# Performance work log

Hardware: AMD Instinct MI355X
Metric: run time of the kernel (lower is better)

Reference implementation:

```python
import jax, jax.numpy as jnp
import numpy as np

NUM_Q = 500000
NUM_E = 250000
DIM = 256
HEADS = 4
NEG_SLOPE = 0.01
EPS = 1e-16


def setup_inputs() -> dict:
    key = jax.random.key(0)
    k1, k2, k3, k4, k5 = jax.random.split(key, 5)
    x_q = jax.random.normal(k1, (NUM_Q, DIM), dtype=jnp.float32)
    x_edge = jax.random.normal(k2, (NUM_E, DIM), dtype=jnp.float32)
    edge_ids = jax.random.randint(k3, (NUM_Q,), 0, NUM_E, dtype=jnp.int64)
    # learned params: w_q (input_dim, output_dim), attention weight (H, 2*dim/H)
    w_q = jax.random.normal(k4, (DIM, DIM), dtype=jnp.float32) / np.sqrt(DIM)
    weight = jax.random.normal(k5, (HEADS, 2 * DIM // HEADS), dtype=jnp.float32) / np.sqrt(2 * DIM // HEADS)
    return {"x_q": x_q, "x_edge": x_edge, "w_q": w_q, "weight": weight, "edge_ids": edge_ids}


def reference(x_q, x_edge, w_q, weight, edge_ids):
    nq = x_q.shape[0]
    ne = x_edge.shape[0]
    h = weight.shape[0]
    # project qualifier pairs: (nq, dim) -> (nq, H, d_head)
    xq = (x_q @ w_q).reshape(nq, h, -1)
    # gather edge reps per qualifier pair: (nq, H, d_head)
    xe = x_edge[edge_ids].reshape(nq, h, -1)
    # per-head attention logits: eh
    alpha = jnp.einsum('ehd,hd->eh', jnp.concatenate([xe, xq], axis=-1), weight)
    alpha = jax.nn.leaky_relu(alpha, NEG_SLOPE)
    # segment softmax grouped by edge_ids (numerically stable)
    seg_max = jax.ops.segment_max(alpha, edge_ids, num_segments=ne)
    seg_max = jnp.where(jnp.isfinite(seg_max), seg_max, 0.0)  # empty segments
    ex = jnp.exp(alpha - seg_max[edge_ids])
    seg_sum = jax.ops.segment_sum(ex, edge_ids, num_segments=ne)
    alpha = ex / (seg_sum[edge_ids] + EPS)
    # weight qualifier reps and scatter-add to edges
    xq = (alpha[..., None] * xq).reshape(nq, -1)
    return jax.ops.segment_sum(xq, edge_ids, num_segments=ne)
```

## Files before the change

kernel.cpp:

```cpp
#include <hip/hip_runtime.h>
#include <hip/hip_bf16.h>

#define DIM 256
#define HEADS 4
#define NEG_SLOPE 0.01f

typedef unsigned short u16;
typedef __attribute__((ext_vector_type(8))) short short8;
typedef __attribute__((ext_vector_type(4))) float f32x4;
typedef __attribute__((ext_vector_type(4))) unsigned short u16x4;

__device__ __forceinline__ u16 f2bf(float f) {
    unsigned u = __float_as_uint(f);
    unsigned r = (u + 0x7fffu + ((u >> 16) & 1u)) >> 16;
    return (u16)r;
}
__device__ __forceinline__ float bf2f(u16 h) {
    return __uint_as_float(((unsigned)h) << 16);
}

__global__ __launch_bounds__(256) void prepb_kernel(const float* __restrict__ B,
                                                    u16* __restrict__ BThi) {
    int k = blockIdx.x;
    int n = threadIdx.x;
    BThi[n * 256 + k] = f2bf(B[k * 256 + n]);
}

__global__ __launch_bounds__(256) void beta_kernel(const float* __restrict__ xe,
                                                   const float* __restrict__ weight,
                                                   float* __restrict__ beta, int NE) {
    int wid = blockIdx.x * 4 + (threadIdx.x >> 6);
    if (wid >= NE) return;
    int lane = threadIdx.x & 63;
    int h = lane >> 4;
    float4 v = *reinterpret_cast<const float4*>(xe + (size_t)wid * DIM + lane * 4);
    float4 w = *reinterpret_cast<const float4*>(weight + h * 128 + (lane & 15) * 4);
    float p = v.x * w.x + v.y * w.y + v.z * w.z + v.w * w.w;
    p += __shfl_xor(p, 1);
    p += __shfl_xor(p, 2);
    p += __shfl_xor(p, 4);
    p += __shfl_xor(p, 8);
    if ((lane & 15) == 0) beta[(size_t)wid * 4 + h] = p;
}

__global__ __launch_bounds__(256, 3) void gemm_fused_kernel(const float* __restrict__ A,
                                                            const u16* __restrict__ BThi,
                                                            const float* __restrict__ weight,
                                                            const float* __restrict__ beta,
                                                            const int* __restrict__ eids,
                                                            u16* __restrict__ xq_out,
                                                            float* __restrict__ exv,
                                                            float* __restrict__ segsum,
                                                            unsigned* __restrict__ counts,
                                                            int NQ) {
    __shared__ u16 Ahi_s[64 * 32];
    __shared__ u16 Bhi_s[256 * 32];

    const int t = threadIdx.x;
    const int lane = t & 63;
    const int wc = t >> 6;
    const int lr = lane & 15;
    const int kg = lane >> 4;
    const long brow = (long)blockIdx.x * 64;

    f32x4 acc[4][4];
#pragma unroll
    for (int m = 0; m < 4; ++m)
#pragma unroll
        for (int n = 0; n < 4; ++n) acc[m][n] = (f32x4){0.f, 0.f, 0.f, 0.f};

    for (int k0 = 0; k0 < DIM; k0 += 32) {
#pragma unroll
        for (int i = 0; i < 2; ++i) {
            int slot = t + i * 256;
            int row = slot >> 3, c4 = slot & 7;
            long grow = brow + row;
            if (grow >= NQ) grow = NQ - 1;
            float4 v = *reinterpret_cast<const float4*>(A + grow * DIM + k0 + c4 * 4);
            u16x4 hv;
            hv.x = f2bf(v.x); hv.y = f2bf(v.y); hv.z = f2bf(v.z); hv.w = f2bf(v.w);
            int swz = (c4 >> 1) ^ (row & 3) ^ ((row >> 2) & 3);
            int off = row * 32 + (swz << 3) + ((c4 & 1) << 2);
            *reinterpret_cast<u16x4*>(&Ahi_s[off]) = hv;
        }
#pragma unroll
        for (int i = 0; i < 4; ++i) {
            int slot = t + i * 256;
            int n = slot >> 2, c = slot & 3;
            uint4 vh = *reinterpret_cast<const uint4*>(BThi + n * 256 + k0 + c * 8);
            int swz = c ^ (n & 3) ^ ((n >> 2) & 3);
            *reinterpret_cast<uint4*>(&Bhi_s[n * 32 + (swz << 3)]) = vh;
        }
        __syncthreads();

        short8 bh[4];
#pragma unroll
        for (int n = 0; n < 4; ++n) {
            int nn = wc * 64 + n * 16 + lr;
            int off = nn * 32 + ((kg ^ (nn & 3) ^ ((nn >> 2) & 3)) << 3);
            bh[n] = *reinterpret_cast<const short8*>(&Bhi_s[off]);
        }
#pragma unroll
        for (int m = 0; m < 4; ++m) {
            int rr = m * 16 + lr;
            int off = rr * 32 + ((kg ^ (rr & 3) ^ ((rr >> 2) & 3)) << 3);
            short8 ah = *reinterpret_cast<const short8*>(&Ahi_s[off]);
#pragma unroll
            for (int n = 0; n < 4; ++n)
                acc[m][n] = __builtin_amdgcn_mfma_f32_16x16x32_bf16(ah, bh[n], acc[m][n], 0, 0, 0);
        }
        __syncthreads();
    }

    float wv[4];
#pragma unroll
    for (int n = 0; n < 4; ++n) wv[n] = weight[wc * 128 + 64 + n * 16 + lr];

#pragma unroll
    for (int m = 0; m < 4; ++m) {
#pragma unroll
        for (int r = 0; r < 4; ++r) {
            long row = brow + m * 16 + kg * 4 + r;
            bool ok = row < NQ;
            float p = 0.f;
#pragma unroll
            for (int n = 0; n < 4; ++n) {
                float v = acc[m][n][r];
                if (ok) xq_out[row * DIM + wc * 64 + n * 16 + lr] = f2bf(v);
                p = fmaf(v, wv[n], p);
            }
            p += __shfl_xor(p, 1);
            p += __shfl_xor(p, 2);
            p += __shfl_xor(p, 4);
            p += __shfl_xor(p, 8);
            if (ok && lr == 0) {
                int j = eids[row];
                float l = beta[(size_t)j * 4 + wc] + p;
                l = l > 0.f ? l : NEG_SLOPE * l;
                float e = __expf(l);
                exv[row * 4 + wc] = e;
                atomicAdd(&segsum[(size_t)j * 4 + wc], e);
                if (wc == 0) atomicAdd(&counts[j], 1u);
            }
        }
    }
}

__global__ __launch_bounds__(256) void scan1_kernel(const unsigned* __restrict__ counts,
                                                    unsigned* __restrict__ offs,
                                                    unsigned* __restrict__ blocksums, int NE) {
    __shared__ unsigned s[256];
    int t = threadIdx.x;
    int base = blockIdx.x * 1024 + t * 4;
    unsigned v[4], sum = 0;
#pragma unroll
    for (int i = 0; i < 4; ++i) {
        v[i] = (base + i < NE) ? counts[base + i] : 0u;
        sum += v[i];
    }
    s[t] = sum;
    __syncthreads();
    for (int off = 1; off < 256; off <<= 1) {
        unsigned y = (t >= off) ? s[t - off] : 0u;
        __syncthreads();
        s[t] += y;
        __syncthreads();
    }
    unsigned excl = s[t] - sum;
#pragma unroll
    for (int i = 0; i < 4; ++i) {
        if (base + i < NE) offs[base + i] = excl;
        excl += v[i];
    }
    if (t == 255) blocksums[blockIdx.x] = s[255];
}

__global__ __launch_bounds__(256) void scan2_kernel(unsigned* __restrict__ blocksums, int NB) {
    __shared__ unsigned s[256];
    int t = threadIdx.x;
    unsigned v = (t < NB) ? blocksums[t] : 0u;
    s[t] = v;
    __syncthreads();
    for (int off = 1; off < 256; off <<= 1) {
        unsigned y = (t >= off) ? s[t - off] : 0u;
        __syncthreads();
        s[t] += y;
        __syncthreads();
    }
    if (t < NB) blocksums[t] = s[t] - v;
}

__global__ __launch_bounds__(256) void scan3_kernel(unsigned* __restrict__ offs,
                                                    const unsigned* __restrict__ blocksums,
                                                    unsigned* __restrict__ cursor, int NE) {
    int t = threadIdx.x;
    int base = blockIdx.x * 1024 + t * 4;
    unsigned add = blocksums[blockIdx.x];
#pragma unroll
    for (int i = 0; i < 4; ++i) {
        if (base + i < NE) {
            unsigned o = offs[base + i] + add;
            offs[base + i] = o;
            cursor[base + i] = o;
        }
    }
}

__global__ __launch_bounds__(256) void fill_kernel(const int* __restrict__ eids,
                                                   unsigned* __restrict__ cursor,
                                                   int* __restrict__ qlist, int NQ) {
    int e = blockIdx.x * blockDim.x + threadIdx.x;
    if (e >= NQ) return;
    int j = eids[e];
    unsigned pos = atomicAdd(&cursor[j], 1u);
    qlist[pos] = e;
}

__global__ __launch_bounds__(256) void gather_kernel(const float* __restrict__ exv,
                                                     const float* __restrict__ segsum,
                                                     const unsigned* __restrict__ offs,
                                                     const unsigned* __restrict__ counts,
                                                     const int* __restrict__ qlist,
                                                     const u16* __restrict__ xq,
                                                     float* __restrict__ out, int NE) {
    int j = blockIdx.x * 4 + (threadIdx.x >> 6);
    if (j >= NE) return;
    int lane = threadIdx.x & 63;
    int h = lane >> 4;
    unsigned beg = offs[j];
    unsigned n = counts[j];
    float inv = 1.0f / (segsum[(size_t)j * 4 + h] + 1e-16f);
    float4 a0 = make_float4(0.f, 0.f, 0.f, 0.f);
    float4 a1 = make_float4(0.f, 0.f, 0.f, 0.f);
    unsigned i = 0;
    for (; i + 2 <= n; i += 2) {
        int q0 = qlist[beg + i];
        int q1 = qlist[beg + i + 1];
        float w0 = exv[(size_t)q0 * 4 + h] * inv;
        float w1 = exv[(size_t)q1 * 4 + h] * inv;
        u16x4 v0 = *reinterpret_cast<const u16x4*>(xq + (size_t)q0 * DIM + lane * 4);
        u16x4 v1 = *reinterpret_cast<const u16x4*>(xq + (size_t)q1 * DIM + lane * 4);
        a0.x = fmaf(w0, bf2f(v0.x), a0.x); a1.x = fmaf(w1, bf2f(v1.x), a1.x);
        a0.y = fmaf(w0, bf2f(v0.y), a0.y); a1.y = fmaf(w1, bf2f(v1.y), a1.y);
        a0.z = fmaf(w0, bf2f(v0.z), a0.z); a1.z = fmaf(w1, bf2f(v1.z), a1.z);
        a0.w = fmaf(w0, bf2f(v0.w), a0.w); a1.w = fmaf(w1, bf2f(v1.w), a1.w);
    }
    if (i < n) {
        int q0 = qlist[beg + i];
        float w0 = exv[(size_t)q0 * 4 + h] * inv;
        u16x4 v0 = *reinterpret_cast<const u16x4*>(xq + (size_t)q0 * DIM + lane * 4);
        a0.x = fmaf(w0, bf2f(v0.x), a0.x);
        a0.y = fmaf(w0, bf2f(v0.y), a0.y);
        a0.z = fmaf(w0, bf2f(v0.z), a0.z);
        a0.w = fmaf(w0, bf2f(v0.w), a0.w);
    }
    float4 acc = make_float4(a0.x + a1.x, a0.y + a1.y, a0.z + a1.z, a0.w + a1.w);
    *reinterpret_cast<float4*>(out + (size_t)j * DIM + lane * 4) = acc;
}

extern "C" void kernel_launch(void* const* d_in, const int* in_sizes, int n_in,
                              void* d_out, int out_size, void* d_ws, size_t ws_size,
                              hipStream_t stream) {
    (void)n_in; (void)out_size; (void)ws_size;
    const float* x_q    = (const float*)d_in[0];
    const float* x_edge = (const float*)d_in[1];
    const float* w_q    = (const float*)d_in[2];
    const float* weight = (const float*)d_in[3];
    const int*   eids   = (const int*)d_in[4];
    const int NQ = in_sizes[0] / DIM;
    const int NE = in_sizes[1] / DIM;
    float* out = (float*)d_out;

    u16*      xq        = (u16*)d_ws;
    float*    exv       = (float*)(xq + (size_t)NQ * DIM);
    float*    beta      = exv + (size_t)NQ * 4;
    float*    segsum    = beta + (size_t)NE * 4;
    unsigned* counts    = (unsigned*)(segsum + (size_t)NE * 4);
    unsigned* offs      = counts + NE;
    unsigned* cursor    = offs + NE;
    int*      qlist     = (int*)(cursor + NE);
    unsigned* blocksums = (unsigned*)(qlist + NQ);
    u16*      BThi      = (u16*)(blocksums + 256);

    const int NB = (NE + 1023) / 1024;

    hipMemsetAsync(segsum, 0, (size_t)NE * 4 * sizeof(float), stream);
    hipMemsetAsync(counts, 0, (size_t)NE * sizeof(unsigned), stream);

    prepb_kernel<<<256, 256, 0, stream>>>(w_q, BThi);
    beta_kernel<<<(NE + 3) / 4, 256, 0, stream>>>(x_edge, weight, beta, NE);
    gemm_fused_kernel<<<(NQ + 63) / 64, 256, 0, stream>>>(x_q, BThi, weight, beta, eids,
                                                          xq, exv, segsum, counts, NQ);
    scan1_kernel<<<NB, 256, 0, stream>>>(counts, offs, blocksums, NE);
    scan2_kernel<<<1, 256, 0, stream>>>(blocksums, NB);
    scan3_kernel<<<NB, 256, 0, stream>>>(offs, blocksums, cursor, NE);
    fill_kernel<<<(NQ + 255) / 256, 256, 0, stream>>>(eids, cursor, qlist, NQ);
    gather_kernel<<<(NE + 3) / 4, 256, 0, stream>>>(exv, segsum, offs, counts, qlist, xq, out, NE);
}
```

Before: 562.7 us.

## Double-buffer GEMM LDS tiles with register prefetch of next K-slice

The fused projection GEMM now prefetches the next K-slice of A and B into registers while running the MFMAs on the current LDS buffer, then writes it into a second LDS buffer. The goal is to hide global load latency behind compute in the 8-step K loop. LDS use doubles (about 40KB per block), which may limit the occupancy of 3 blocks per CU, and registers rise because of the prefetch buffers. The loop still keeps two barriers per step.

```diff
diff --git a/kernel.cpp b/kernel.cpp
--- a/kernel.cpp
+++ b/kernel.cpp
@@ -53,8 +53,8 @@
                                                             float* __restrict__ segsum,
                                                             unsigned* __restrict__ counts,
                                                             int NQ) {
-    __shared__ u16 Ahi_s[64 * 32];
-    __shared__ u16 Bhi_s[256 * 32];
+    __shared__ u16 A_s[2][64 * 32];
+    __shared__ u16 B_s[2][256 * 32];
 
     const int t = threadIdx.x;
     const int lane = t & 63;
@@ -63,53 +63,81 @@
     const int kg = lane >> 4;
     const long brow = (long)blockIdx.x * 64;
 
+    const int a_row = t >> 3, a_c4 = t & 7;
+    const int b_n = t >> 2, b_c = t & 3;
+
     f32x4 acc[4][4];
 #pragma unroll
     for (int m = 0; m < 4; ++m)
 #pragma unroll
         for (int n = 0; n < 4; ++n) acc[m][n] = (f32x4){0.f, 0.f, 0.f, 0.f};
 
-    for (int k0 = 0; k0 < DIM; k0 += 32) {
+    float4 a_reg[2];
+    uint4  b_reg[4];
+
+    auto load_tile = [&](int k0) {
 #pragma unroll
         for (int i = 0; i < 2; ++i) {
-            int slot = t + i * 256;
-            int row = slot >> 3, c4 = slot & 7;
-            long grow = brow + row;
+            long grow = brow + a_row + i * 32;
             if (grow >= NQ) grow = NQ - 1;
-            float4 v = *reinterpret_cast<const float4*>(A + grow * DIM + k0 + c4 * 4);
+            a_reg[i] = *reinterpret_cast<const float4*>(A + grow * DIM + k0 + a_c4 * 4);
+        }
+#pragma unroll
+        for (int i = 0; i < 4; ++i) {
+            int n = b_n + i * 64;
+            b_reg[i] = *reinterpret_cast<const uint4*>(BThi + n * 256 + k0 + b_c * 8);
+        }
+    };
+    auto write_tile = [&](int buf) {
+#pragma unroll
+        for (int i = 0; i < 2; ++i) {
+            int row = a_row + i * 32;
+            float4 v = a_reg[i];
             u16x4 hv;
             hv.x = f2bf(v.x); hv.y = f2bf(v.y); hv.z = f2bf(v.z); hv.w = f2bf(v.w);
-            int swz = (c4 >> 1) ^ (row & 3) ^ ((row >> 2) & 3);
-            int off = row * 32 + (swz << 3) + ((c4 & 1) << 2);
-            *reinterpret_cast<u16x4*>(&Ahi_s[off]) = hv;
+            int swz = (a_c4 >> 1) ^ (row & 3) ^ ((row >> 2) & 3);
+            int off = row * 32 + (swz << 3) + ((a_c4 & 1) << 2);
+            *reinterpret_cast<u16x4*>(&A_s[buf][off]) = hv;
         }
 #pragma unroll
         for (int i = 0; i < 4; ++i) {
-            int slot = t + i * 256;
-            int n = slot >> 2, c = slot & 3;
-            uint4 vh = *reinterpret_cast<const uint4*>(BThi + n * 256 + k0 + c * 8);
-            int swz = c ^ (n & 3) ^ ((n >> 2) & 3);
-            *reinterpret_cast<uint4*>(&Bhi_s[n * 32 + (swz << 3)]) = vh;
-        }
-        __syncthreads();
+            int n = b_n + i * 64;
+            int swz = b_c ^ (n & 3) ^ ((n >> 2) & 3);
+            *reinterpret_cast<uint4*>(&B_s[buf][n * 32 + (swz << 3)]) = b_reg[i];
+        }
+    };
+
+    load_tile(0);
+    write_tile(0);
+    __syncthreads();
+
+#pragma unroll
+    for (int step = 0; step < 8; ++step) {
+        const int buf = step & 1;
+        if (step < 7) load_tile((step + 1) * 32);
 
         short8 bh[4];
 #pragma unroll
         for (int n = 0; n < 4; ++n) {
             int nn = wc * 64 + n * 16 + lr;
             int off = nn * 32 + ((kg ^ (nn & 3) ^ ((nn >> 2) & 3)) << 3);
-            bh[n] = *reinterpret_cast<const short8*>(&Bhi_s[off]);
+            bh[n] = *reinterpret_cast<const short8*>(&B_s[buf][off]);
         }
 #pragma unroll
         for (int m = 0; m < 4; ++m) {
             int rr = m * 16 + lr;
             int off = rr * 32 + ((kg ^ (rr & 3) ^ ((rr >> 2) & 3)) << 3);
-            short8 ah = *reinterpret_cast<const short8*>(&Ahi_s[off]);
+            short8 ah = *reinterpret_cast<const short8*>(&A_s[buf][off]);
 #pragma unroll
             for (int n = 0; n < 4; ++n)
                 acc[m][n] = __builtin_amdgcn_mfma_f32_16x16x32_bf16(ah, bh[n], acc[m][n], 0, 0, 0);
         }
-        __syncthreads();
+
+        if (step < 7) {
+            __syncthreads();
+            write_tile(buf ^ 1);
+            __syncthreads();
+        }
     }
 
     float wv[4];
```

New measurement: 732.6 us. +30.2%, slower.

## Load A fragments directly into registers, bypassing LDS, and prefetch B before barrier

Applied to the files above, without the earlier changes.

The GEMM kernel no longer stages the A tile through shared memory. Each lane loads the fp32 A elements its MFMA fragment needs straight from global memory and converts them to bf16 in registers. B global loads are issued into registers before the first barrier and then written to LDS, and the trailing barrier is dropped so the loop uses a different barrier pattern. This removes the A LDS round trip and one sync per k-step, at the cost of more register use and less coalesced A loads (32-byte chunks per lane across 16 rows).

```diff
diff --git a/kernel.cpp b/kernel.cpp
--- a/kernel.cpp
+++ b/kernel.cpp
@@ -17,6 +17,9 @@
 }
 __device__ __forceinline__ float bf2f(u16 h) {
     return __uint_as_float(((unsigned)h) << 16);
+}
+__device__ __forceinline__ unsigned pack2bf(float a, float b) {
+    return (unsigned)f2bf(a) | ((unsigned)f2bf(b) << 16);
 }
 
 __global__ __launch_bounds__(256) void prepb_kernel(const float* __restrict__ B,
@@ -53,8 +56,7 @@
                                                             float* __restrict__ segsum,
                                                             unsigned* __restrict__ counts,
                                                             int NQ) {
-    __shared__ u16 Ahi_s[64 * 32];
-    __shared__ u16 Bhi_s[256 * 32];
+    __shared__ u16 B_s[256 * 32];
 
     const int t = threadIdx.x;
     const int lane = t & 63;
@@ -63,6 +65,16 @@
     const int kg = lane >> 4;
     const long brow = (long)blockIdx.x * 64;
 
+    const int b_n = t >> 2, b_c = t & 3;
+
+    const float* arow[4];
+#pragma unroll
+    for (int m = 0; m < 4; ++m) {
+        long grow = brow + m * 16 + lr;
+        if (grow >= NQ) grow = NQ - 1;
+        arow[m] = A + grow * DIM + kg * 8;
+    }
+
     f32x4 acc[4][4];
 #pragma unroll
     for (int m = 0; m < 4; ++m)
@@ -70,26 +82,25 @@
         for (int n = 0; n < 4; ++n) acc[m][n] = (f32x4){0.f, 0.f, 0.f, 0.f};
 
     for (int k0 = 0; k0 < DIM; k0 += 32) {
-#pragma unroll
-        for (int i = 0; i < 2; ++i) {
-            int slot = t + i * 256;
-            int row = slot >> 3, c4 = slot & 7;
-            long grow = brow + row;
-            if (grow >= NQ) grow = NQ - 1;
-            float4 v = *reinterpret_cast<const float4*>(A + grow * DIM + k0 + c4 * 4);
-            u16x4 hv;
-            hv.x = f2bf(v.x); hv.y = f2bf(v.y); hv.z = f2bf(v.z); hv.w = f2bf(v.w);
-            int swz = (c4 >> 1) ^ (row & 3) ^ ((row >> 2) & 3);
-            int off = row * 32 + (swz << 3) + ((c4 & 1) << 2);
-            *reinterpret_cast<u16x4*>(&Ahi_s[off]) = hv;
-        }
+        uint4 vb[4];
 #pragma unroll
         for (int i = 0; i < 4; ++i) {
-            int slot = t + i * 256;
-            int n = slot >> 2, c = slot & 3;
-            uint4 vh = *reinterpret_cast<const uint4*>(BThi + n * 256 + k0 + c * 8);
-            int swz = c ^ (n & 3) ^ ((n >> 2) & 3);
-            *reinterpret_cast<uint4*>(&Bhi_s[n * 32 + (swz << 3)]) = vh;
+            int n = b_n + i * 64;
+            vb[i] = *reinterpret_cast<const uint4*>(BThi + n * 256 + k0 + b_c * 8);
+        }
+        float4 af[4][2];
+#pragma unroll
+        for (int m = 0; m < 4; ++m) {
+            af[m][0] = *reinterpret_cast<const float4*>(arow[m] + k0);
+            af[m][1] = *reinterpret_cast<const float4*>(arow[m] + k0 + 4);
+        }
+
+        __syncthreads();
+#pragma unroll
+        for (int i = 0; i < 4; ++i) {
+            int n = b_n + i * 64;
+            int swz = b_c ^ (n & 3) ^ ((n >> 2) & 3);
+            *reinterpret_cast<uint4*>(&B_s[n * 32 + (swz << 3)]) = vb[i];
         }
         __syncthreads();
 
@@ -98,18 +109,20 @@
         for (int n = 0; n < 4; ++n) {
             int nn = wc * 64 + n * 16 + lr;
             int off = nn * 32 + ((kg ^ (nn & 3) ^ ((nn >> 2) & 3)) << 3);
-            bh[n] = *reinterpret_cast<const short8*>(&Bhi_s[off]);
+            bh[n] = *reinterpret_cast<const short8*>(&B_s[off]);
         }
 #pragma unroll
         for (int m = 0; m < 4; ++m) {
-            int rr = m * 16 + lr;
-            int off = rr * 32 + ((kg ^ (rr & 3) ^ ((rr >> 2) & 3)) << 3);
-            short8 ah = *reinterpret_cast<const short8*>(&Ahi_s[off]);
+            unsigned p0 = pack2bf(af[m][0].x, af[m][0].y);
+            unsigned p1 = pack2bf(af[m][0].z, af[m][0].w);
+            unsigned p2 = pack2bf(af[m][1].x, af[m][1].y);
+            unsigned p3 = pack2bf(af[m][1].z, af[m][1].w);
+            uint4 packed = make_uint4(p0, p1, p2, p3);
+            short8 ah = *reinterpret_cast<short8*>(&packed);
 #pragma unroll
             for (int n = 0; n < 4; ++n)
                 acc[m][n] = __builtin_amdgcn_mfma_f32_16x16x32_bf16(ah, bh[n], acc[m][n], 0, 0, 0);
         }
-        __syncthreads();
     }
 
     float wv[4];
```

Result: slower. 995.2 us (+76.9%).

## Double-buffer A tile in LDS and load B fragments directly from global

Applied to the files above, without the earlier changes.

The GEMM loop now prefetches the next A slice into registers while running MFMAs on the current slice. It writes that slice into a second LDS buffer, so each k-step needs one barrier instead of two. The B (weight) tile is no longer staged through LDS; each wave reads its bf16 fragments straight from global memory, which should hit in cache because the 256x256 matrix is small. This cuts LDS traffic and synchronisation, at the cost of extra global/L2 reads for B and more live registers.

```diff
diff --git a/kernel.cpp b/kernel.cpp
--- a/kernel.cpp
+++ b/kernel.cpp
@@ -53,8 +53,7 @@
                                                             float* __restrict__ segsum,
                                                             unsigned* __restrict__ counts,
                                                             int NQ) {
-    __shared__ u16 Ahi_s[64 * 32];
-    __shared__ u16 Bhi_s[256 * 32];
+    __shared__ u16 A_s[2][64 * 32];
 
     const int t = threadIdx.x;
     const int lane = t & 63;
@@ -63,53 +62,72 @@
     const int kg = lane >> 4;
     const long brow = (long)blockIdx.x * 64;
 
+    const int s_row0 = t >> 3, s_c4 = t & 7;
+    const float* aptr0;
+    const float* aptr1;
+    {
+        long g0 = brow + s_row0;       if (g0 >= NQ) g0 = NQ - 1;
+        long g1 = brow + s_row0 + 32;  if (g1 >= NQ) g1 = NQ - 1;
+        aptr0 = A + g0 * DIM + s_c4 * 4;
+        aptr1 = A + g1 * DIM + s_c4 * 4;
+    }
+    const u16* brows[4];
+#pragma unroll
+    for (int n = 0; n < 4; ++n)
+        brows[n] = BThi + (wc * 64 + n * 16 + lr) * 256 + kg * 8;
+
     f32x4 acc[4][4];
 #pragma unroll
     for (int m = 0; m < 4; ++m)
 #pragma unroll
         for (int n = 0; n < 4; ++n) acc[m][n] = (f32x4){0.f, 0.f, 0.f, 0.f};
 
-    for (int k0 = 0; k0 < DIM; k0 += 32) {
+    float4 a_reg0, a_reg1;
+    auto load_a = [&](int k0) {
+        a_reg0 = *reinterpret_cast<const float4*>(aptr0 + k0);
+        a_reg1 = *reinterpret_cast<const float4*>(aptr1 + k0);
+    };
+    auto write_a = [&](int buf) {
 #pragma unroll
         for (int i = 0; i < 2; ++i) {
-            int slot = t + i * 256;
-            int row = slot >> 3, c4 = slot & 7;
-            long grow = brow + row;
-            if (grow >= NQ) grow = NQ - 1;
-            float4 v = *reinterpret_cast<const float4*>(A + grow * DIM + k0 + c4 * 4);
+            int row = s_row0 + i * 32;
+            float4 v = i ? a_reg1 : a_reg0;
             u16x4 hv;
             hv.x = f2bf(v.x); hv.y = f2bf(v.y); hv.z = f2bf(v.z); hv.w = f2bf(v.w);
-            int swz = (c4 >> 1) ^ (row & 3) ^ ((row >> 2) & 3);
-            int off = row * 32 + (swz << 3) + ((c4 & 1) << 2);
-            *reinterpret_cast<u16x4*>(&Ahi_s[off]) = hv;
-        }
-#pragma unroll
-        for (int i = 0; i < 4; ++i) {
-            int slot = t + i * 256;
-            int n = slot >> 2, c = slot & 3;
-            uint4 vh = *reinterpret_cast<const uint4*>(BThi + n * 256 + k0 + c * 8);
-            int swz = c ^ (n & 3) ^ ((n >> 2) & 3);
-            *reinterpret_cast<uint4*>(&Bhi_s[n * 32 + (swz << 3)]) = vh;
-        }
-        __syncthreads();
+            int swz = (s_c4 >> 1) ^ (row & 3) ^ ((row >> 2) & 3);
+            int off = row * 32 + (swz << 3) + ((s_c4 & 1) << 2);
+            *reinterpret_cast<u16x4*>(&A_s[buf][off]) = hv;
+        }
+    };
+
+    load_a(0);
+    write_a(0);
+    __syncthreads();
+
+    for (int step = 0; step < 8; ++step) {
+        const int buf = step & 1;
+        const int k0 = step * 32;
+        if (step < 7) load_a(k0 + 32);
 
         short8 bh[4];
 #pragma unroll
-        for (int n = 0; n < 4; ++n) {
-            int nn = wc * 64 + n * 16 + lr;
-            int off = nn * 32 + ((kg ^ (nn & 3) ^ ((nn >> 2) & 3)) << 3);
-            bh[n] = *reinterpret_cast<const short8*>(&Bhi_s[off]);
-        }
+        for (int n = 0; n < 4; ++n)
+            bh[n] = *reinterpret_cast<const short8*>(brows[n] + k0);
+
 #pragma unroll
         for (int m = 0; m < 4; ++m) {
             int rr = m * 16 + lr;
             int off = rr * 32 + ((kg ^ (rr & 3) ^ ((rr >> 2) & 3)) << 3);
-            short8 ah = *reinterpret_cast<const short8*>(&Ahi_s[off]);
+            short8 ah = *reinterpret_cast<const short8*>(&A_s[buf][off]);
 #pragma unroll
             for (int n = 0; n < 4; ++n)
                 acc[m][n] = __builtin_amdgcn_mfma_f32_16x16x32_bf16(ah, bh[n], acc[m][n], 0, 0, 0);
         }
-        __syncthreads();
+
+        if (step < 7) {
+            write_a(buf ^ 1);
+            __syncthreads();
+        }
     }
 
     float wv[4];
```

Measured after the change: 561.9 us. Within noise of the previous version (-0.1%).
